# Kernel tuning notes

Measured on AMD Instinct MI355X. Metric: run time of the kernel, lower is better.

Reference implementation:

```python
import jax, jax.numpy as jnp
import numpy as np

GAMMA = 2.0  # args.gamma
B, C, H, W = 8, 21, 512, 512


def setup_inputs() -> dict:
    key = jax.random.key(0)
    k1, k2 = jax.random.split(key)
    pred = jax.random.normal(k1, (B, C, H, W), dtype=jnp.float32)
    # one-hot target built from random per-pixel class labels
    labels = jax.random.randint(k2, (B, H, W), 0, C)
    target = jax.nn.one_hot(labels, C, dtype=jnp.float32)  # [B,H,W,C]
    target = jnp.transpose(target, (0, 3, 1, 2))  # [B,C,H,W]
    return {"pred": pred, "target": target}


def reference(pred, target) -> jnp.ndarray:
    b, c, h, w = pred.shape
    logits = jax.nn.log_softmax(pred, axis=1)  # [B,C,H,W]
    lo = jnp.transpose(logits, (0, 2, 3, 1)).reshape(-1, c)  # [N,C]
    tg = jnp.transpose(target, (0, 2, 3, 1)).reshape(-1, c)  # [N,C]
    n = lo.shape[0]
    beta = (n - 1.0) / n
    # per-pixel focal term summed over channels: sum_j (1-p_j)^gamma * log p_j * t_j
    row_val = jnp.sum((1.0 - jnp.exp(lo)) ** GAMMA * lo * tg, axis=1)  # [N]
    mask = (tg == 1).astype(lo.dtype)  # [N,C] class membership mask
    n_c = jnp.sum(mask, axis=0)  # [C] pixels per class
    class_sum = jnp.einsum('nc,n->c', mask, row_val)  # [C] masked reductions
    w = (1.0 - beta) / (1.0 - jnp.power(jnp.float32(beta), n_c) + 1e-6)  # [C]
    return -jnp.sum(w * class_sum) / n
```

## Files before the change

### kernel.cpp

```cpp
#include <hip/hip_runtime.h>

#define BBATCH 8
#define CCH    21
#define HWSZ   (512*512)
#define HW4    (HWSZ/4)
#define NPIX   (BBATCH*HWSZ)
#define BLKT   256
#define NBLK   (NPIX/4/BLKT)

__global__ void cb_zero(float* __restrict__ acc) {
    if (threadIdx.x < 2 * CCH) acc[threadIdx.x] = 0.f;
}

__global__ __launch_bounds__(BLKT) void cb_focal_partial(
    const float4* __restrict__ pred4, const float4* __restrict__ targ4,
    float* __restrict__ gsum, float* __restrict__ gcnt)
{
    __shared__ float ls_sum[CCH];
    __shared__ float ls_cnt[CCH];
    if (threadIdx.x < CCH) { ls_sum[threadIdx.x] = 0.f; ls_cnt[threadIdx.x] = 0.f; }
    __syncthreads();

    const int tid = blockIdx.x * BLKT + threadIdx.x;
    const int b   = tid >> 16;
    const int hw4 = tid & (HW4 - 1);
    const float4* pp = pred4 + (size_t)b * CCH * HW4 + hw4;
    const float4* tp = targ4 + (size_t)b * CCH * HW4 + hw4;

    float s0 = 0.f, s1 = 0.f, s2 = 0.f, s3 = 0.f;
    float vy0 = 0.f, vy1 = 0.f, vy2 = 0.f, vy3 = 0.f;
    float ey0 = 1.f, ey1 = 1.f, ey2 = 1.f, ey3 = 1.f;
    int   y0 = 0, y1 = 0, y2 = 0, y3 = 0;

    #pragma unroll
    for (int c = 0; c < CCH; ++c) {
        const float4 v = pp[(size_t)c * HW4];
        const float4 t = tp[(size_t)c * HW4];
        const float e0 = __expf(v.x), e1 = __expf(v.y),
                    e2 = __expf(v.z), e3 = __expf(v.w);
        s0 += e0; s1 += e1; s2 += e2; s3 += e3;
        const bool h0 = t.x > 0.5f, h1 = t.y > 0.5f,
                   h2 = t.z > 0.5f, h3 = t.w > 0.5f;
        y0 = h0 ? c : y0;  vy0 = h0 ? v.x : vy0;  ey0 = h0 ? e0 : ey0;
        y1 = h1 ? c : y1;  vy1 = h1 ? v.y : vy1;  ey1 = h1 ? e1 : ey1;
        y2 = h2 ? c : y2;  vy2 = h2 ? v.z : vy2;  ey2 = h2 ? e2 : ey2;
        y3 = h3 ? c : y3;  vy3 = h3 ? v.w : vy3;  ey3 = h3 ? e3 : ey3;
    }

    {
        const float l0 = vy0 - __logf(s0), p0 = ey0 / s0, o0 = 1.f - p0;
        const float l1 = vy1 - __logf(s1), p1 = ey1 / s1, o1 = 1.f - p1;
        const float l2 = vy2 - __logf(s2), p2 = ey2 / s2, o2 = 1.f - p2;
        const float l3 = vy3 - __logf(s3), p3 = ey3 / s3, o3 = 1.f - p3;
        atomicAdd(&ls_sum[y0], o0 * o0 * l0);  atomicAdd(&ls_cnt[y0], 1.f);
        atomicAdd(&ls_sum[y1], o1 * o1 * l1);  atomicAdd(&ls_cnt[y1], 1.f);
        atomicAdd(&ls_sum[y2], o2 * o2 * l2);  atomicAdd(&ls_cnt[y2], 1.f);
        atomicAdd(&ls_sum[y3], o3 * o3 * l3);  atomicAdd(&ls_cnt[y3], 1.f);
    }
    __syncthreads();
    if (threadIdx.x < CCH) {
        atomicAdd(&gsum[threadIdx.x], ls_sum[threadIdx.x]);
        atomicAdd(&gcnt[threadIdx.x], ls_cnt[threadIdx.x]);
    }
}

__global__ void cb_focal_final(const float* __restrict__ gsum,
                               const float* __restrict__ gcnt,
                               float* __restrict__ out)
{
    const int lane = threadIdx.x;
    double term = 0.0;
    if (lane < CCH) {
        const double n    = (double)NPIX;
        const double beta = (n - 1.0) / n;
        const double w = (1.0 - beta) / (1.0 - pow(beta, (double)gcnt[lane]) + 1e-6);
        term = w * (double)gsum[lane];
    }
    for (int off = 32; off; off >>= 1) term += __shfl_down(term, off, 64);
    if (lane == 0) out[0] = (float)(-term / (double)NPIX);
}

extern "C" void kernel_launch(void* const* d_in, const int* in_sizes, int n_in,
                              void* d_out, int out_size, void* d_ws, size_t ws_size,
                              hipStream_t stream) {
    const float4* pred4 = (const float4*)d_in[0];
    const float4* targ4 = (const float4*)d_in[1];
    float* out  = (float*)d_out;
    float* gsum = (float*)d_ws;
    float* gcnt = gsum + CCH;

    cb_zero<<<1, 64, 0, stream>>>(gsum);
    cb_focal_partial<<<NBLK, BLKT, 0, stream>>>(pred4, targ4, gsum, gcnt);
    cb_focal_final<<<1, 64, 0, stream>>>(gsum, gcnt, out);
}
```

Before: 359.0 us.

## Stage channel loads into LDS with double-buffered async global_load_lds pipeline

Replaces direct float4 global loads with global_load_lds, which writes channel batches of pred and target into a double-buffered LDS ring. The next batch is issued while the current one is computed, with explicit vmcnt waits and sched barriers. The goal is to keep more memory requests in flight on a bandwidth-bound streaming kernel. It also swaps the zeroing kernel for hipMemsetAsync, and adds 48KB of LDS per block, which may reduce occupancy.

```diff
diff --git a/kernel.cpp b/kernel.cpp
--- a/kernel.cpp
+++ b/kernel.cpp
@@ -1,21 +1,30 @@
 #include <hip/hip_runtime.h>
 
-#define BBATCH 8
 #define CCH    21
 #define HWSZ   (512*512)
 #define HW4    (HWSZ/4)
-#define NPIX   (BBATCH*HWSZ)
+#define NPIX   (8*HWSZ)
 #define BLKT   256
 #define NBLK   (NPIX/4/BLKT)
+#define CB     3
+#define NBATCH (CCH/CB)
 
-__global__ void cb_zero(float* __restrict__ acc) {
-    if (threadIdx.x < 2 * CCH) acc[threadIdx.x] = 0.f;
+#define WAIT_VM6() __builtin_amdgcn_s_waitcnt(0x0F70 | 6)
+#define WAIT_VM0() __builtin_amdgcn_s_waitcnt(0x0F70 | 0)
+
+typedef float vfloat4 __attribute__((ext_vector_type(4)));
+
+__device__ __forceinline__ void stage16(const float* g, vfloat4* l) {
+    __builtin_amdgcn_global_load_lds(
+        (const __attribute__((address_space(1))) unsigned int*)g,
+        (__attribute__((address_space(3))) unsigned int*)l, 16, 0, 0);
 }
 
 __global__ __launch_bounds__(BLKT) void cb_focal_partial(
-    const float4* __restrict__ pred4, const float4* __restrict__ targ4,
+    const float* __restrict__ pred, const float* __restrict__ targ,
     float* __restrict__ gsum, float* __restrict__ gcnt)
 {
+    __shared__ vfloat4 sbuf[2][2*CB][BLKT];
     __shared__ float ls_sum[CCH];
     __shared__ float ls_cnt[CCH];
     if (threadIdx.x < CCH) { ls_sum[threadIdx.x] = 0.f; ls_cnt[threadIdx.x] = 0.f; }
@@ -24,28 +33,55 @@
     const int tid = blockIdx.x * BLKT + threadIdx.x;
     const int b   = tid >> 16;
     const int hw4 = tid & (HW4 - 1);
-    const float4* pp = pred4 + (size_t)b * CCH * HW4 + hw4;
-    const float4* tp = targ4 + (size_t)b * CCH * HW4 + hw4;
+    const float* pp = pred + (size_t)b * CCH * HWSZ + (size_t)hw4 * 4;
+    const float* tp = targ + (size_t)b * CCH * HWSZ + (size_t)hw4 * 4;
+    const int wv = threadIdx.x & 192;
 
     float s0 = 0.f, s1 = 0.f, s2 = 0.f, s3 = 0.f;
     float vy0 = 0.f, vy1 = 0.f, vy2 = 0.f, vy3 = 0.f;
     float ey0 = 1.f, ey1 = 1.f, ey2 = 1.f, ey3 = 1.f;
     int   y0 = 0, y1 = 0, y2 = 0, y3 = 0;
 
+    auto issue = [&](int k, int buf) {
+        #pragma unroll
+        for (int j = 0; j < CB; ++j) {
+            const size_t coff = (size_t)(k * CB + j) * HWSZ;
+            stage16(pp + coff, &sbuf[buf][2*j    ][wv]);
+            stage16(tp + coff, &sbuf[buf][2*j + 1][wv]);
+        }
+    };
+
+    auto compute = [&](int k) {
+        #pragma unroll
+        for (int j = 0; j < CB; ++j) {
+            const vfloat4 v = sbuf[k & 1][2*j    ][threadIdx.x];
+            const vfloat4 t = sbuf[k & 1][2*j + 1][threadIdx.x];
+            const int c = k * CB + j;
+            const float e0 = __expf(v.x), e1 = __expf(v.y),
+                        e2 = __expf(v.z), e3 = __expf(v.w);
+            s0 += e0; s1 += e1; s2 += e2; s3 += e3;
+            const bool h0 = t.x > 0.5f, h1 = t.y > 0.5f,
+                       h2 = t.z > 0.5f, h3 = t.w > 0.5f;
+            y0 = h0 ? c : y0;  vy0 = h0 ? v.x : vy0;  ey0 = h0 ? e0 : ey0;
+            y1 = h1 ? c : y1;  vy1 = h1 ? v.y : vy1;  ey1 = h1 ? e1 : ey1;
+            y2 = h2 ? c : y2;  vy2 = h2 ? v.z : vy2;  ey2 = h2 ? e2 : ey2;
+            y3 = h3 ? c : y3;  vy3 = h3 ? v.w : vy3;  ey3 = h3 ? e3 : ey3;
+        }
+    };
+
+    issue(0, 0);
     #pragma unroll
-    for (int c = 0; c < CCH; ++c) {
-        const float4 v = pp[(size_t)c * HW4];
-        const float4 t = tp[(size_t)c * HW4];
-        const float e0 = __expf(v.x), e1 = __expf(v.y),
-                    e2 = __expf(v.z), e3 = __expf(v.w);
-        s0 += e0; s1 += e1; s2 += e2; s3 += e3;
-        const bool h0 = t.x > 0.5f, h1 = t.y > 0.5f,
-                   h2 = t.z > 0.5f, h3 = t.w > 0.5f;
-        y0 = h0 ? c : y0;  vy0 = h0 ? v.x : vy0;  ey0 = h0 ? e0 : ey0;
-        y1 = h1 ? c : y1;  vy1 = h1 ? v.y : vy1;  ey1 = h1 ? e1 : ey1;
-        y2 = h2 ? c : y2;  vy2 = h2 ? v.z : vy2;  ey2 = h2 ? e2 : ey2;
-        y3 = h3 ? c : y3;  vy3 = h3 ? v.w : vy3;  ey3 = h3 ? e3 : ey3;
+    for (int k = 0; k < NBATCH - 1; ++k) {
+        issue(k + 1, (k + 1) & 1);
+        __builtin_amdgcn_sched_barrier(0);
+        WAIT_VM6();
+        __builtin_amdgcn_sched_barrier(0);
+        compute(k);
     }
+    __builtin_amdgcn_sched_barrier(0);
+    WAIT_VM0();
+    __builtin_amdgcn_sched_barrier(0);
+    compute(NBATCH - 1);
 
     {
         const float l0 = vy0 - __logf(s0), p0 = ey0 / s0, o0 = 1.f - p0;
@@ -83,13 +119,13 @@
 extern "C" void kernel_launch(void* const* d_in, const int* in_sizes, int n_in,
                               void* d_out, int out_size, void* d_ws, size_t ws_size,
                               hipStream_t stream) {
-    const float4* pred4 = (const float4*)d_in[0];
-    const float4* targ4 = (const float4*)d_in[1];
+    const float* pred = (const float*)d_in[0];
+    const float* targ = (const float*)d_in[1];
     float* out  = (float*)d_out;
     float* gsum = (float*)d_ws;
     float* gcnt = gsum + CCH;
 
-    cb_zero<<<1, 64, 0, stream>>>(gsum);
-    cb_focal_partial<<<NBLK, BLKT, 0, stream>>>(pred4, targ4, gsum, gcnt);
+    (void)hipMemsetAsync(gsum, 0, 2 * CCH * sizeof(float), stream);
+    cb_focal_partial<<<NBLK, BLKT, 0, stream>>>(pred, targ, gsum, gcnt);
     cb_focal_final<<<1, 64, 0, stream>>>(gsum, gcnt, out);
 }
```

New measurement: 358.4 us. Within noise of the previous version (-0.2%).
